# Optimization experiments

Measured on AMD Instinct MI355X. Metric: run time of the kernel, lower is better.

## Reference

```python
import jax, jax.numpy as jnp
import numpy as np

IN_C, C_M, C_N, K = 512, 512, 128, 1
B, H, W = 8, 64, 64

def setup_inputs() -> dict:
    key = jax.random.key(0)
    ks = jax.random.split(key, 8)
    s = 1.0 / np.sqrt(IN_C)
    return {
        "x": jax.random.normal(ks[0], (B, IN_C, H, W), dtype=jnp.float32),
        "y": jax.random.normal(ks[1], (B, C_M, H, W), dtype=jnp.float32),
        "wA": jax.random.uniform(ks[2], (C_M, IN_C), minval=-s, maxval=s, dtype=jnp.float32),
        "bA": jax.random.uniform(ks[3], (C_M,), minval=-s, maxval=s, dtype=jnp.float32),
        "wB": jax.random.uniform(ks[4], (C_N, IN_C), minval=-s, maxval=s, dtype=jnp.float32),
        "bB": jax.random.uniform(ks[5], (C_N,), minval=-s, maxval=s, dtype=jnp.float32),
        "wV": jax.random.uniform(ks[6], (C_N, IN_C), minval=-s, maxval=s, dtype=jnp.float32),
        "bV": jax.random.uniform(ks[7], (C_N,), minval=-s, maxval=s, dtype=jnp.float32),
    }

def reference(x, y, wA, bA, wB, bB, wV, bV):
    # A2-Net double attention, K=1 so batch = b1 and K*h*w = N.
    b, c, h, w = x.shape
    N = h * w
    xf = x.reshape(b, c, N)                                  # [b, C, N]
    A = jnp.einsum('mc,bcn->bmn', wA, xf) + bA[:, None]      # [b, c_m, N]
    Bf = jnp.einsum('kc,bcn->bkn', wB, xf) + bB[:, None]     # [b, c_n, N]
    V = jnp.einsum('kc,bcn->bkn', wV, xf) + bV[:, None]      # [b, c_n, N]
    # tmpB viewed (b*c_n, N), softmax dim=1 -> softmax over N per (b, c_n) row
    softB = jax.nn.softmax(Bf, axis=-1)                      # [b, c_n, N]
    # tmpV viewed (b*N, c_n), softmax dim=1 -> softmax over c_n per pixel
    softV = jax.nn.softmax(V, axis=1)                        # [b, c_n, N]
    # gather: tmpG = tmpA @ softB^T  -> [b, c_m, c_n]
    G = jnp.einsum('bmn,bkn->bmk', A, softB)
    # distribute: tmpZ = G @ softV -> [b, c_m, N]
    Z = jnp.einsum('bmk,bkn->bmn', G, softV)
    return Z.reshape(b, -1, h, w) + y
```

## Files before the change

kernel.cpp:

```cpp
#include <hip/hip_runtime.h>

#define BATCH 8
#define INC 512
#define CM 512
#define CN 128
#define NPIX 4096
#define NSPLIT 8

typedef short bf16x8 __attribute__((ext_vector_type(8)));
typedef float f32x4 __attribute__((ext_vector_type(4)));
typedef unsigned short us8v __attribute__((ext_vector_type(8)));

__device__ __forceinline__ unsigned short f2b(float f) {
    union { float f; unsigned u; } v; v.f = f;
    unsigned r = v.u + 0x7FFF + ((v.u >> 16) & 1);
    return (unsigned short)(r >> 16);
}
__device__ __forceinline__ float b2f(unsigned short u) {
    union { unsigned u; float f; } v; v.u = ((unsigned)u) << 16;
    return v.f;
}

__device__ __forceinline__ void gl_lds16(const unsigned short* g, unsigned short* l) {
    __builtin_amdgcn_global_load_lds(
        (const __attribute__((address_space(1))) unsigned int*)g,
        (__attribute__((address_space(3))) unsigned int*)l, 16, 0, 0);
}

__device__ __forceinline__ void stage_tile(const unsigned short* src, int ld, int kbase,
                                           unsigned short* lds, int t) {
    #pragma unroll
    for (int q = 0; q < 2; ++q) {
        int f = q * 256 + t;
        const unsigned short* g = src + (size_t)(f >> 2) * ld + kbase + (f & 3) * 8;
        gl_lds16(g, lds + f * 8);
    }
}

__device__ __forceinline__ void stage_half(const unsigned short* src, int ld, int kbase,
                                           unsigned short* lds, int t) {
    const unsigned short* g = src + (size_t)(t >> 2) * ld + kbase + (t & 3) * 8;
    gl_lds16(g, lds + t * 8);
}

__device__ __forceinline__ void bt_compute(const unsigned short* lA, const unsigned short* lB,
                                           f32x4 acc[4][4], int wr, int wc, int lane) {
    int lr = lane & 15, lq = lane >> 4;
    bf16x8 av[4], bv[4];
    #pragma unroll
    for (int i = 0; i < 4; ++i)
        av[i] = *(const bf16x8*)&lA[(wr * 64 + i * 16 + lr) * 32 + lq * 8];
    #pragma unroll
    for (int j = 0; j < 4; ++j)
        bv[j] = *(const bf16x8*)&lB[(wc * 64 + j * 16 + lr) * 32 + lq * 8];
    #pragma unroll
    for (int i = 0; i < 4; ++i)
        #pragma unroll
        for (int j = 0; j < 4; ++j)
            acc[i][j] = __builtin_amdgcn_mfma_f32_16x16x32_bf16(av[i], bv[j], acc[i][j], 0, 0, 0);
}

__device__ __forceinline__ void bt2_compute(const unsigned short* lA0, const unsigned short* lA1,
                                            const unsigned short* lBx,
                                            f32x4 aB[4][2], f32x4 aV[4][2],
                                            int wr, int wc, int lane) {
    int lr = lane & 15, lq = lane >> 4;
    bf16x8 a0[4], a1[4], bv[2];
    #pragma unroll
    for (int i = 0; i < 4; ++i) {
        a0[i] = *(const bf16x8*)&lA0[(wr * 64 + i * 16 + lr) * 32 + lq * 8];
        a1[i] = *(const bf16x8*)&lA1[(wr * 64 + i * 16 + lr) * 32 + lq * 8];
    }
    #pragma unroll
    for (int j = 0; j < 2; ++j)
        bv[j] = *(const bf16x8*)&lBx[(wc * 32 + j * 16 + lr) * 32 + lq * 8];
    #pragma unroll
    for (int i = 0; i < 4; ++i)
        #pragma unroll
        for (int j = 0; j < 2; ++j) {
            aB[i][j] = __builtin_amdgcn_mfma_f32_16x16x32_bf16(a0[i], bv[j], aB[i][j], 0, 0, 0);
            aV[i][j] = __builtin_amdgcn_mfma_f32_16x16x32_bf16(a1[i], bv[j], aV[i][j], 0, 0, 0);
        }
}

#define ZERO_ACC(acc)                       \
    f32x4 acc[4][4];                        \
    {                                       \
        f32x4 z4 = {0.f, 0.f, 0.f, 0.f};   \
        for (int i = 0; i < 4; ++i)         \
            for (int j = 0; j < 4; ++j)     \
                acc[i][j] = z4;             \
    }

__device__ __forceinline__ void pipe_loop(const unsigned short* A, int lda,
                                          const unsigned short* Bm, int ldb,
                                          int kbase, int nt,
                                          unsigned short* lds, f32x4 acc[4][4],
                                          int t, int wr, int wc, int lane)
{
    stage_tile(A, lda, kbase, lds, t);
    stage_tile(Bm, ldb, kbase, lds + 4096, t);
    __syncthreads();
    int cur = 0;
    for (int it = 0; it < nt - 1; ++it) {
        unsigned short* nb = lds + ((cur ^ 1) << 13);
        stage_tile(A, lda, kbase + (it + 1) * 32, nb, t);
        stage_tile(Bm, ldb, kbase + (it + 1) * 32, nb + 4096, t);
        bt_compute(lds + (cur << 13), lds + (cur << 13) + 4096, acc, wr, wc, lane);
        __syncthreads();
        cur ^= 1;
    }
    bt_compute(lds + (cur << 13), lds + (cur << 13) + 4096, acc, wr, wc, lane);
}

__global__ __launch_bounds__(256) void k_prep(
    const float* __restrict__ x, const float* __restrict__ wA,
    const float* __restrict__ wB, const float* __restrict__ wV,
    unsigned short* __restrict__ xT, unsigned short* __restrict__ x16,
    unsigned short* __restrict__ wA16, unsigned short* __restrict__ wB16,
    unsigned short* __restrict__ wV16)
{
    if (blockIdx.z == BATCH) {
        int bl = blockIdx.y * 64 + blockIdx.x;
        if (bl >= 384) return;
        int e = (bl * 256 + threadIdx.x) * 4;
        const float* src; unsigned short* dst; int off;
        if (e < 262144)       { src = wA; dst = wA16; off = e; }
        else if (e < 327680)  { src = wB; dst = wB16; off = e - 262144; }
        else                  { src = wV; dst = wV16; off = e - 327680; }
        float4 v = *(const float4*)&src[off];
        *(ushort4*)&dst[off] = make_ushort4(f2b(v.x), f2b(v.y), f2b(v.z), f2b(v.w));
        return;
    }
    __shared__ unsigned short tile[64][68];
    int n0 = blockIdx.x * 64, c0 = blockIdx.y * 64, b = blockIdx.z;
    int t = threadIdx.x;
    int tr = t >> 4, tc4 = (t & 15) * 4;
    const float* xb = x + ((size_t)b * INC + c0) * NPIX + n0;
    unsigned short* x16p = x16 + ((size_t)b * INC + c0) * NPIX + n0;
    #pragma unroll
    for (int p = 0; p < 4; ++p) {
        int r = p * 16 + tr;
        float4 v = *(const float4*)&xb[(size_t)r * NPIX + tc4];
        ushort4 u = make_ushort4(f2b(v.x), f2b(v.y), f2b(v.z), f2b(v.w));
        *(ushort4*)&x16p[(size_t)r * NPIX + tc4] = u;
        tile[r][tc4 + 0] = u.x; tile[r][tc4 + 1] = u.y;
        tile[r][tc4 + 2] = u.z; tile[r][tc4 + 3] = u.w;
    }
    __syncthreads();
    unsigned short* o = xT + ((size_t)b * NPIX + n0) * INC + c0;
    #pragma unroll
    for (int p = 0; p < 4; ++p) {
        int n = p * 16 + tr;
        ushort4 u = make_ushort4(tile[tc4 + 0][n], tile[tc4 + 1][n],
                                 tile[tc4 + 2][n], tile[tc4 + 3][n]);
        *(ushort4*)&o[(size_t)n * INC + tc4] = u;
    }
}

__global__ __launch_bounds__(256) void k_proj(
    const unsigned short* __restrict__ xT, const unsigned short* __restrict__ wB16,
    const unsigned short* __restrict__ wV16, const float* __restrict__ bB,
    const float* __restrict__ bV, unsigned short* __restrict__ Bf16,
    unsigned short* __restrict__ V16)
{
    __shared__ __align__(16) unsigned short lds[20480];
    int t = threadIdx.x;
    int n0 = blockIdx.x * 64, b = blockIdx.y;
    const unsigned short* Bx = xT + ((size_t)b * NPIX + n0) * INC;

    f32x4 accB[4][2], accV[4][2];
    {
        f32x4 z4 = {0.f, 0.f, 0.f, 0.f};
        for (int i = 0; i < 4; ++i)
            for (int j = 0; j < 2; ++j) { accB[i][j] = z4; accV[i][j] = z4; }
    }
    int lane = t & 63, w = t >> 6, wr = w >> 1, wc = w & 1;
    int lr = lane & 15, lq = lane >> 4;

    stage_tile(wB16, INC, 0, lds, t);
    stage_tile(wV16, INC, 0, lds + 4096, t);
    stage_half(Bx, INC, 0, lds + 8192, t);
    __syncthreads();
    int cur = 0;
    for (int it = 0; it < 15; ++it) {
        unsigned short* nb = lds + (cur ^ 1) * 10240;
        int c = (it + 1) * 32;
        stage_tile(wB16, INC, c, nb, t);
        stage_tile(wV16, INC, c, nb + 4096, t);
        stage_half(Bx, INC, c, nb + 8192, t);
        const unsigned short* cb = lds + cur * 10240;
        bt2_compute(cb, cb + 4096, cb + 8192, accB, accV, wr, wc, lane);
        __syncthreads();
        cur ^= 1;
    }
    {
        const unsigned short* cb = lds + cur * 10240;
        bt2_compute(cb, cb + 4096, cb + 8192, accB, accV, wr, wc, lane);
    }
    int r0 = wr * 64 + lq * 4;
    #pragma unroll
    for (int i = 0; i < 4; ++i)
        #pragma unroll
        for (int reg = 0; reg < 4; ++reg) {
            int k = r0 + i * 16 + reg;
            float vB = bB[k], vV = bV[k];
            size_t rowo = ((size_t)b * CN + k) * NPIX + n0 + wc * 32 + lr;
            #pragma unroll
            for (int j = 0; j < 2; ++j) {
                Bf16[rowo + j * 16] = f2b(accB[i][j][reg] + vB);
                V16 [rowo + j * 16] = f2b(accV[i][j][reg] + vV);
            }
        }
}

__global__ __launch_bounds__(256) void k_softmax_rows(
    const unsigned short* __restrict__ Bf16, unsigned short* __restrict__ sB)
{
    __shared__ float red[8];
    int row = blockIdx.x, t = threadIdx.x;
    const unsigned short* p = Bf16 + (size_t)row * NPIX + t * 16;
    us8v u0 = *(const us8v*)p, u1 = *(const us8v*)(p + 8);
    float v[16];
    #pragma unroll
    for (int j = 0; j < 8; ++j) { v[j] = b2f(u0[j]); v[8 + j] = b2f(u1[j]); }
    float m = -1e30f;
    #pragma unroll
    for (int j = 0; j < 16; ++j) m = fmaxf(m, v[j]);
    for (int o = 32; o > 0; o >>= 1) m = fmaxf(m, __shfl_xor(m, o));
    if ((t & 63) == 0) red[t >> 6] = m;
    __syncthreads();
    m = fmaxf(fmaxf(red[0], red[1]), fmaxf(red[2], red[3]));
    float s = 0.f;
    #pragma unroll
    for (int j = 0; j < 16; ++j) { v[j] = __expf(v[j] - m); s += v[j]; }
    for (int o = 32; o > 0; o >>= 1) s += __shfl_xor(s, o);
    if ((t & 63) == 0) red[4 + (t >> 6)] = s;
    __syncthreads();
    float r = 1.0f / (red[4] + red[5] + red[6] + red[7]);
    us8v o0, o1;
    #pragma unroll
    for (int j = 0; j < 8; ++j) { o0[j] = f2b(v[j] * r); o1[j] = f2b(v[8 + j] * r); }
    unsigned short* q = sB + (size_t)row * NPIX + t * 16;
    *(us8v*)q = o0; *(us8v*)(q + 8) = o1;
}

__global__ __launch_bounds__(256) void k_softmax_cols(
    const unsigned short* __restrict__ V16, unsigned short* __restrict__ sVt)
{
    __shared__ unsigned short tv[128][138];
    __shared__ float pm[2][128], ps[2][128], sm[128], sr[128];
    int n0 = blockIdx.x * 128, b = blockIdx.y, t = threadIdx.x;
    const unsigned short* vb = V16 + (size_t)b * CN * NPIX + n0;
    #pragma unroll
    for (int it = 0; it < 8; ++it) {
        int f = it * 256 + t, k = f >> 4, n8 = (f & 15) * 8;
        us8v u = *(const us8v*)&vb[(size_t)k * NPIX + n8];
        #pragma unroll
        for (int j = 0; j < 8; ++j) tv[n8 + j][k] = u[j];
    }
    __syncthreads();
    {
        int p = t & 127, h = t >> 7;
        float m = -1e30f;
        for (int k = h * 64; k < h * 64 + 64; ++k) m = fmaxf(m, b2f(tv[p][k]));
        float s = 0.f;
        for (int k = h * 64; k < h * 64 + 64; ++k) s += __expf(b2f(tv[p][k]) - m);
        pm[h][p] = m; ps[h][p] = s;
    }
    __syncthreads();
    if (t < 128) {
        float ma = pm[0][t], mb = pm[1][t];
        float m = fmaxf(ma, mb);
        float s = ps[0][t] * __expf(ma - m) + ps[1][t] * __expf(mb - m);
        sm[t] = m; sr[t] = 1.0f / s;
    }
    __syncthreads();
    unsigned short* ob = sVt + ((size_t)b * NPIX + n0) * CN;
    #pragma unroll
    for (int it = 0; it < 8; ++it) {
        int idx = it * 2048 + t * 8, nl = idx >> 7, k0 = idx & 127;
        float m = sm[nl], r = sr[nl];
        us8v o;
        #pragma unroll
        for (int j = 0; j < 8; ++j) o[j] = f2b(__expf(b2f(tv[nl][k0 + j]) - m) * r);
        *(us8v*)&ob[(size_t)nl * CN + k0] = o;
    }
}

__global__ __launch_bounds__(256) void k_gather(
    const unsigned short* __restrict__ x16, const unsigned short* __restrict__ sB,
    float* __restrict__ Pts)
{
    __shared__ __align__(16) unsigned short lds[16384];
    int t = threadIdx.x;
    int c0 = blockIdx.x * 128, s = blockIdx.y, b = blockIdx.z;
    const unsigned short* A = sB + (size_t)b * CN * NPIX;
    const unsigned short* Bm = x16 + ((size_t)b * INC + c0) * NPIX;
    int nbase = s * (NPIX / NSPLIT);

    ZERO_ACC(acc);
    int lane = t & 63, w = t >> 6, wr = w >> 1, wc = w & 1;

    pipe_loop(A, NPIX, Bm, NPIX, nbase, (NPIX / NSPLIT) / 32, lds, acc, t, wr, wc, lane);

    int lr = lane & 15, lq = lane >> 4;
    int r0 = wr * 64 + lq * 4;
    float* op = Pts + ((size_t)s * BATCH + b) * CN * INC + c0 + wc * 64 + lr;
    #pragma unroll
    for (int i = 0; i < 4; ++i)
        #pragma unroll
        for (int reg = 0; reg < 4; ++reg) {
            int k = r0 + i * 16 + reg;
            #pragma unroll
            for (int j = 0; j < 4; ++j)
                op[(size_t)k * INC + j * 16] = acc[i][j][reg];
        }
}

__global__ __launch_bounds__(256) void k_reduceP(
    const float* __restrict__ Pts, unsigned short* __restrict__ Pt16)
{
    int base = (blockIdx.x * 256 + threadIdx.x) * 4;
    float4 sacc = make_float4(0.f, 0.f, 0.f, 0.f);
    #pragma unroll
    for (int sp = 0; sp < NSPLIT; ++sp) {
        float4 v = *(const float4*)&Pts[(size_t)sp * (BATCH * CN * INC) + base];
        sacc.x += v.x; sacc.y += v.y; sacc.z += v.z; sacc.w += v.w;
    }
    *(ushort4*)&Pt16[base] = make_ushort4(f2b(sacc.x), f2b(sacc.y), f2b(sacc.z), f2b(sacc.w));
}

__global__ __launch_bounds__(256) void k_G(
    const unsigned short* __restrict__ wA16, const float* __restrict__ bA,
    const unsigned short* __restrict__ Pt16, unsigned short* __restrict__ G16)
{
    __shared__ __align__(16) unsigned short lds[16384];
    int t = threadIdx.x;
    int m0 = blockIdx.x * 128, b = blockIdx.y;
    const unsigned short* A = wA16 + (size_t)m0 * INC;
    const unsigned short* Bm = Pt16 + (size_t)b * CN * INC;

    ZERO_ACC(acc);
    int lane = t & 63, w = t >> 6, wr = w >> 1, wc = w & 1;

    pipe_loop(A, INC, Bm, INC, 0, INC / 32, lds, acc, t, wr, wc, lane);

    int lr = lane & 15, lq = lane >> 4;
    int r0 = wr * 64 + lq * 4;
    unsigned short* op = G16 + ((size_t)b * CM + m0) * CN + wc * 64 + lr;
    #pragma unroll
    for (int i = 0; i < 4; ++i)
        #pragma unroll
        for (int reg = 0; reg < 4; ++reg) {
            int mloc = r0 + i * 16 + reg;
            float bv_ = bA[m0 + mloc];
            #pragma unroll
            for (int j = 0; j < 4; ++j)
                op[(size_t)mloc * CN + j * 16] = f2b(acc[i][j][reg] + bv_);
        }
}

__global__ __launch_bounds__(256) void k_Z(
    const unsigned short* __restrict__ G16, const unsigned short* __restrict__ sVt,
    const float* __restrict__ y, float* __restrict__ out)
{
    __shared__ __align__(16) unsigned short lds[16384];
    int t = threadIdx.x;
    int n0 = blockIdx.x * 128, m0 = blockIdx.y * 128, b = blockIdx.z;
    const unsigned short* A = G16 + ((size_t)b * CM + m0) * CN;
    const unsigned short* Bm = sVt + ((size_t)b * NPIX + n0) * CN;

    ZERO_ACC(acc);
    int lane = t & 63, w = t >> 6, wr = w >> 1, wc = w & 1;
    int lr = lane & 15, lq = lane >> 4;
    size_t rbase = ((size_t)b * CM + m0 + wr * 64 + lq * 4) * NPIX + n0 + wc * 64 + lr;

    stage_tile(A, CN, 0, lds, t);
    stage_tile(Bm, CN, 0, lds + 4096, t);
    float yA[2][4][4];
    #pragma unroll
    for (int i = 0; i < 2; ++i)
        #pragma unroll
        for (int reg = 0; reg < 4; ++reg)
            #pragma unroll
            for (int j = 0; j < 4; ++j)
                yA[i][reg][j] = y[rbase + (size_t)(i * 16 + reg) * NPIX + j * 16];
    __syncthreads();
    int cur = 0;
    for (int it = 0; it < 3; ++it) {
        unsigned short* nb = lds + ((cur ^ 1) << 13);
        stage_tile(A, CN, (it + 1) * 32, nb, t);
        stage_tile(Bm, CN, (it + 1) * 32, nb + 4096, t);
        bt_compute(lds + (cur << 13), lds + (cur << 13) + 4096, acc, wr, wc, lane);
        __syncthreads();
        cur ^= 1;
    }
    bt_compute(lds + (cur << 13), lds + (cur << 13) + 4096, acc, wr, wc, lane);

    #pragma unroll
    for (int i = 0; i < 2; ++i)
        #pragma unroll
        for (int reg = 0; reg < 4; ++reg) {
            size_t ro = rbase + (size_t)(i * 16 + reg) * NPIX;
            #pragma unroll
            for (int j = 0; j < 4; ++j)
                out[ro + j * 16] = acc[i][j][reg] + yA[i][reg][j];
        }
    #pragma unroll
    for (int i = 2; i < 4; ++i)
        #pragma unroll
        for (int reg = 0; reg < 4; ++reg) {
            size_t ro = rbase + (size_t)(i * 16 + reg) * NPIX;
            #pragma unroll
            for (int j = 0; j < 4; ++j)
                out[ro + j * 16] = acc[i][j][reg] + y[ro + j * 16];
        }
}

extern "C" void kernel_launch(void* const* d_in, const int* in_sizes, int n_in,
                              void* d_out, int out_size, void* d_ws, size_t ws_size,
                              hipStream_t stream)
{
    const float* x  = (const float*)d_in[0];
    const float* y  = (const float*)d_in[1];
    const float* wA = (const float*)d_in[2];
    const float* bA = (const float*)d_in[3];
    const float* wB = (const float*)d_in[4];
    const float* bB = (const float*)d_in[5];
    const float* wV = (const float*)d_in[6];
    const float* bV = (const float*)d_in[7];
    float* out = (float*)d_out;

    unsigned short* xT16 = (unsigned short*)d_ws;
    unsigned short* x16  = xT16 + 16777216;
    unsigned short* wA16 = x16  + 16777216;
    unsigned short* wB16 = wA16 + 262144;
    unsigned short* wV16 = wB16 + 65536;
    unsigned short* Bf16 = wV16 + 65536;
    unsigned short* V16  = Bf16 + 4194304;
    unsigned short* sB   = V16  + 4194304;
    unsigned short* sVt  = sB   + 4194304;
    unsigned short* Pt16 = sVt  + 4194304;
    float*  Pts = (float*)(Pt16 + 524288);
    unsigned short* G16  = (unsigned short*)(Pts + (size_t)NSPLIT * BATCH * CN * INC);

    k_prep<<<dim3(64, 8, BATCH + 1), 256, 0, stream>>>(
        x, wA, wB, wV, xT16, x16, wA16, wB16, wV16);
    k_proj<<<dim3(NPIX / 64, BATCH), 256, 0, stream>>>(
        xT16, wB16, wV16, bB, bV, Bf16, V16);
    k_softmax_rows<<<dim3(BATCH * CN), 256, 0, stream>>>(Bf16, sB);
    k_softmax_cols<<<dim3(NPIX / 128, BATCH), 256, 0, stream>>>(V16, sVt);
    k_gather<<<dim3(INC / 128, NSPLIT, BATCH), 256, 0, stream>>>(x16, sB, Pts);
    k_reduceP<<<512, 256, 0, stream>>>(Pts, Pt16);
    k_G<<<dim3(CM / 128, BATCH), 256, 0, stream>>>(wA16, bA, Pt16, G16);
    k_Z<<<dim3(NPIX / 128, CM / 128, BATCH), 256, 0, stream>>>(G16, sVt, y, out);
}
```

Measured before the change: 253.7 us.

## Retile k_Z to 32x512 blocks with LDS-staged coalesced float4 epilogue

Changes the Z GEMM tile from 128x128 to 32 rows by 512 pixels per block. Each wave now covers 32x128 outputs. The epilogue stages accumulators through LDS so the y read and the output write use fully coalesced float4 accesses along pixel rows, replacing scattered scalar stores. This targets the memory-bound y/out traffic, which dominates k_Z. The cost is extra LDS traffic and barriers, plus more reloading of sVt across the larger number of m-blocks.

```diff
diff --git a/kernel.cpp b/kernel.cpp
--- a/kernel.cpp
+++ b/kernel.cpp
@@ -365,57 +365,94 @@
     const unsigned short* __restrict__ G16, const unsigned short* __restrict__ sVt,
     const float* __restrict__ y, float* __restrict__ out)
 {
-    __shared__ __align__(16) unsigned short lds[16384];
+    __shared__ __align__(16) unsigned short lds[2 * 17408];
     int t = threadIdx.x;
-    int n0 = blockIdx.x * 128, m0 = blockIdx.y * 128, b = blockIdx.z;
+    int n0 = blockIdx.x * 512, m0 = blockIdx.y * 32, b = blockIdx.z;
     const unsigned short* A = G16 + ((size_t)b * CM + m0) * CN;
     const unsigned short* Bm = sVt + ((size_t)b * NPIX + n0) * CN;
-
-    ZERO_ACC(acc);
-    int lane = t & 63, w = t >> 6, wr = w >> 1, wc = w & 1;
-    int lr = lane & 15, lq = lane >> 4;
-    size_t rbase = ((size_t)b * CM + m0 + wr * 64 + lq * 4) * NPIX + n0 + wc * 64 + lr;
-
-    stage_tile(A, CN, 0, lds, t);
-    stage_tile(Bm, CN, 0, lds + 4096, t);
-    float yA[2][4][4];
-    #pragma unroll
-    for (int i = 0; i < 2; ++i)
-        #pragma unroll
-        for (int reg = 0; reg < 4; ++reg)
-            #pragma unroll
-            for (int j = 0; j < 4; ++j)
-                yA[i][reg][j] = y[rbase + (size_t)(i * 16 + reg) * NPIX + j * 16];
+    int lane = t & 63, w = t >> 6;
+    int lr = lane & 15, lq = lane >> 4;
+
+    f32x4 acc[2][8];
+    {
+        f32x4 z4 = {0.f, 0.f, 0.f, 0.f};
+        for (int i = 0; i < 2; ++i)
+            for (int j = 0; j < 8; ++j) acc[i][j] = z4;
+    }
+
+    #define ZSTAGE(kc, base)                                                      \
+        do {                                                                      \
+            if (t < 128) {                                                        \
+                const unsigned short* g = A + (size_t)(t >> 2) * CN + (kc) + (t & 3) * 8; \
+                gl_lds16(g, (base) + t * 8);                                      \
+            }                                                                     \
+            _Pragma("unroll")                                                     \
+            for (int q = 0; q < 8; ++q) {                                         \
+                int f = q * 256 + t;                                              \
+                const unsigned short* g = Bm + (size_t)(f >> 2) * CN + (kc) + (f & 3) * 8; \
+                gl_lds16(g, (base) + 1024 + f * 8);                               \
+            }                                                                     \
+        } while (0)
+
+    #define ZCOMPUTE(base)                                                        \
+        do {                                                                      \
+            const unsigned short* lA = (base);                                    \
+            const unsigned short* lB = (base) + 1024;                             \
+            bf16x8 av[2], bv[8];                                                  \
+            _Pragma("unroll")                                                     \
+            for (int i = 0; i < 2; ++i)                                           \
+                av[i] = *(const bf16x8*)&lA[(i * 16 + lr) * 32 + lq * 8];         \
+            _Pragma("unroll")                                                     \
+            for (int j = 0; j < 8; ++j)                                           \
+                bv[j] = *(const bf16x8*)&lB[(w * 128 + j * 16 + lr) * 32 + lq * 8]; \
+            _Pragma("unroll")                                                     \
+            for (int i = 0; i < 2; ++i)                                           \
+                _Pragma("unroll")                                                 \
+                for (int j = 0; j < 8; ++j)                                       \
+                    acc[i][j] = __builtin_amdgcn_mfma_f32_16x16x32_bf16(av[i], bv[j], acc[i][j], 0, 0, 0); \
+        } while (0)
+
+    ZSTAGE(0, lds);
     __syncthreads();
     int cur = 0;
     for (int it = 0; it < 3; ++it) {
-        unsigned short* nb = lds + ((cur ^ 1) << 13);
-        stage_tile(A, CN, (it + 1) * 32, nb, t);
-        stage_tile(Bm, CN, (it + 1) * 32, nb + 4096, t);
-        bt_compute(lds + (cur << 13), lds + (cur << 13) + 4096, acc, wr, wc, lane);
+        unsigned short* nb = lds + (cur ^ 1) * 17408;
+        ZSTAGE((it + 1) * 32, nb);
+        ZCOMPUTE(lds + cur * 17408);
         __syncthreads();
         cur ^= 1;
     }
-    bt_compute(lds + (cur << 13), lds + (cur << 13) + 4096, acc, wr, wc, lane);
-
-    #pragma unroll
-    for (int i = 0; i < 2; ++i)
-        #pragma unroll
-        for (int reg = 0; reg < 4; ++reg) {
-            size_t ro = rbase + (size_t)(i * 16 + reg) * NPIX;
+    ZCOMPUTE(lds + cur * 17408);
+
+    float* ep = (float*)lds;
+    size_t obase = ((size_t)b * CM + m0) * NPIX + n0;
+    #pragma unroll
+    for (int p = 0; p < 4; ++p) {
+        __syncthreads();
+        int i = p >> 1, lqa = (p & 1) * 2;
+        if ((lq >> 1) == (p & 1)) {
+            int rloc = (lq - lqa) * 4;
             #pragma unroll
-            for (int j = 0; j < 4; ++j)
-                out[ro + j * 16] = acc[i][j][reg] + yA[i][reg][j];
-        }
-    #pragma unroll
-    for (int i = 2; i < 4; ++i)
-        #pragma unroll
-        for (int reg = 0; reg < 4; ++reg) {
-            size_t ro = rbase + (size_t)(i * 16 + reg) * NPIX;
-            #pragma unroll
-            for (int j = 0; j < 4; ++j)
-                out[ro + j * 16] = acc[i][j][reg] + y[ro + j * 16];
-        }
+            for (int j = 0; j < 8; ++j)
+                #pragma unroll
+                for (int reg = 0; reg < 4; ++reg)
+                    ep[(rloc + reg) * 512 + w * 128 + j * 16 + lr] = acc[i][j][reg];
+        }
+        __syncthreads();
+        size_t gbase = obase + (size_t)(p * 8) * NPIX;
+        #pragma unroll
+        for (int q = 0; q < 4; ++q) {
+            int pi = q * 256 + t;
+            int row = pi >> 7, col = (pi & 127) * 4;
+            size_t go = gbase + (size_t)row * NPIX + col;
+            float4 a = *(const float4*)&ep[row * 512 + col];
+            float4 yv = *(const float4*)&y[go];
+            a.x += yv.x; a.y += yv.y; a.z += yv.z; a.w += yv.w;
+            *(float4*)&out[go] = a;
+        }
+    }
+    #undef ZSTAGE
+    #undef ZCOMPUTE
 }
 
 extern "C" void kernel_launch(void* const* d_in, const int* in_sizes, int n_in,
@@ -454,5 +491,5 @@
     k_gather<<<dim3(INC / 128, NSPLIT, BATCH), 256, 0, stream>>>(x16, sB, Pts);
     k_reduceP<<<512, 256, 0, stream>>>(Pts, Pt16);
     k_G<<<dim3(CM / 128, BATCH), 256, 0, stream>>>(wA16, bA, Pt16, G16);
-    k_Z<<<dim3(NPIX / 128, CM / 128, BATCH), 256, 0, stream>>>(G16, sVt, y, out);
-}
+    k_Z<<<dim3(NPIX / 512, CM / 32, BATCH), 256, 0, stream>>>(G16, sVt, y, out);
+}
```

Result: slower. 261.5 us (+3.1%).
